# Kernel optimization log

Hardware: AMD Instinct MI355X
Metric: run time of the kernel (lower is better)

## Reference

```python
import jax, jax.numpy as jnp
import numpy as np

B, N, C, D, E, VOC, T = 128, 49, 2048, 512, 512, 10000, 20


def setup_inputs() -> dict:
    key = jax.random.key(0)
    ks = jax.random.split(key, 24)
    rn = lambda k, s: (jax.random.normal(k, s) * 0.02).astype(jnp.float32)
    z = lambda s: jnp.zeros(s, dtype=jnp.float32)
    return {
        "image_feature": jax.random.normal(ks[0], (B, N, C), dtype=jnp.float32),
        "target": jax.random.randint(ks[1], (B, T), 0, VOC),
        "emb": rn(ks[2], (VOC, E)),
        "Wa": rn(ks[3], (D, C)), "ba": z((D,)),
        "Wb": rn(ks[4], (D, C)), "bb": z((D,)),
        "Whi": rn(ks[5], (D, C)), "bhi": z((D,)),
        "Wmi": rn(ks[6], (D, C)), "bmi": z((D,)),
        "Wih": rn(ks[7], (4 * D, D + E)), "bih": z((4 * D,)),
        "Whh": rn(ks[8], (4 * D, D)), "bhh": z((4 * D,)),
        "Wv": rn(ks[9], (N, D)),
        "Wg": rn(ks[10], (N, D)),
        "wh": rn(ks[11], (1, N)),
        "WH": rn(ks[12], (D, D)),
        "Wx": rn(ks[13], (D, D + E)),
        "Wh2": rn(ks[14], (D, D)),
        "Ws": rn(ks[15], (N, D)),
        "Wc": rn(ks[16], (D, D)), "bc": z((D,)),
        "Wfc": rn(ks[17], (D, D)), "bfc": z((D,)),
        "Wp": rn(ks[18], (VOC, D)), "bp": z((VOC,)),
    }


def _forward(image_feature, target, emb, Wa, ba, Wb, bb, Whi, bhi, Wmi, bmi,
             Wih, bih, Whh, bhh, Wv, Wg, wh, WH, Wx, Wh2, Ws, Wc, bc,
             Wfc, bfc, Wp, bp):
    relu, sig = jax.nn.relu, jax.nn.sigmoid
    Vf = relu(jnp.einsum('bnc,dc->bnd', image_feature, Wa) + ba)  # [B,N,D]
    mean = image_feature.mean(axis=1)                             # [B,C]
    vg = relu(mean @ Wb.T + bb)                                   # [B,D]
    h0 = relu(mean @ Whi.T + bhi)
    m0 = relu(mean @ Wmi.T + bmi)
    zbase = jnp.einsum('bnd,kd->bnk', Vf, Wv)                     # [B,N,N], fixed per image

    we = emb[target]                                              # [B,T,E]
    we = jnp.concatenate([jnp.zeros((we.shape[0], 1, we.shape[2]), we.dtype), we[:, :-1]], axis=1)
    we_t = jnp.swapaxes(we, 0, 1)                                 # [T,B,E]

    def step(carry, wemb):
        h, m = carry
        x = jnp.concatenate([vg, wemb], axis=1)                   # [B,D+E]
        hp = h
        gates = x @ Wih.T + bih + h @ Whh.T + bhh
        i, f, g, o = jnp.split(gates, 4, axis=1)
        m2 = sig(f) * m + sig(i) * jnp.tanh(g)
        h2 = sig(o) * jnp.tanh(m2)
        H = relu(h2 @ WH.T)                                       # [B,D]
        gH = H @ Wg.T                                             # [B,N]
        z = jnp.squeeze(jnp.tanh(zbase + gH[:, None, :]) @ wh.T, -1)  # [B,N]
        gt = sig(x @ Wx.T + hp @ Wh2.T)                           # [B,D]
        s = relu((gt * jnp.tanh(m2)) @ Wc.T + bc)                 # [B,D]
        z2 = jnp.tanh(s @ Ws.T + gH) @ wh.T                       # [B,1]
        alpha = jax.nn.softmax(jnp.concatenate([z, z2], axis=1), axis=1)  # [B,N+1]
        ctx = jnp.einsum('bn,bnd->bd', alpha[:, :-1], Vf) + alpha[:, -1:] * s
        out = jnp.tanh((H + ctx) @ Wfc.T + bfc)
        logit = out @ Wp.T + bp                                   # [B,VOC]
        return (h2, m2), (logit, alpha[:, :-1])

    _, (logits, attn) = jax.lax.scan(step, (h0, m0), we_t)
    logits = jnp.swapaxes(logits, 0, 1)                           # [B,T,VOC]
    attn = jnp.swapaxes(attn, 0, 1)                               # [B,T,N]
    return jax.nn.log_softmax(logits, axis=2), attn


def reference(image_feature, target, emb, Wa, ba, Wb, bb, Whi, bhi, Wmi, bmi,
              Wih, bih, Whh, bhh, Wv, Wg, wh, WH, Wx, Wh2, Ws, Wc, bc,
              Wfc, bfc, Wp, bp):
    return _forward(image_feature, target, emb, Wa, ba, Wb, bb, Whi, bhi,
                    Wmi, bmi, Wih, bih, Whh, bhh, Wv, Wg, wh, WH, Wx, Wh2,
                    Ws, Wc, bc, Wfc, bfc, Wp, bp)
```

## Files before the change

### kernel.cpp

```cpp
#include <hip/hip_runtime.h>
#include <hip/hip_bf16.h>

static const int kB = 128, kN = 49, kC = 2048, kD = 512, kE = 512, kV = 10000, kT = 20;

typedef __bf16 bf16x8 __attribute__((ext_vector_type(8)));
typedef float  f32x4v __attribute__((ext_vector_type(4)));
typedef _Float16 h8_t __attribute__((ext_vector_type(8)));
typedef _Float16 h2v_t __attribute__((ext_vector_type(2)));
typedef unsigned short u16;
typedef unsigned int u32;

#if defined(__has_builtin)
#if __has_builtin(__builtin_amdgcn_fdot2)
#define HAS_FDOT2 1
#endif
#endif
#ifndef HAS_FDOT2
#define HAS_FDOT2 0
#endif

#define AS1 __attribute__((address_space(1)))
#define AS3 __attribute__((address_space(3)))

__device__ __forceinline__ float sigmoidf_(float x){ return 1.f/(1.f+expf(-x)); }
__device__ __forceinline__ u16 f2b(float x){ __hip_bfloat16 h = __float2bfloat16(x); return *(u16*)&h; }
__device__ __forceinline__ float bu2f(u32 u){ u32 w = u << 16; union{u32 u; float f;} c; c.u = w; return c.f; }

#define TBM 128
#define TBN 128
#define TBK 32

__global__ __launch_bounds__(256) void gemm_bf16(
    const u16* __restrict__ A, int lda,
    const u16* __restrict__ W, int ldw,
    float* __restrict__ C, u16* __restrict__ Cbf, int ldc,
    int M, int N, int K,
    const float* __restrict__ bias,
    const float* __restrict__ add1, int ld1, int a1mask,
    int act,
    const u16* __restrict__ mul2, int ldm,
    int swz)
{
    __shared__ __align__(16) u16 As[TBM*TBK];
    __shared__ __align__(16) u16 Bs[TBN*TBK];
    const int tid = threadIdx.x;
    int bm, bn;
    if (swz){
        const int mblocks = (M + TBM - 1)/TBM;
        const int per_g = mblocks*8;
        const int id = blockIdx.x;
        const int g = id/per_g, r = id - g*per_g;
        bm = (r >> 3)*TBM;
        bn = (g*8 + (r & 7))*TBN;
        if (bn >= N) return;
    } else {
        bm = blockIdx.y * TBM;
        bn = blockIdx.x * TBN;
    }
    const int wave = tid >> 6, lane = tid & 63;
    const int wm = (wave >> 1) * 64, wn = (wave & 1) * 64;
    const int lm = lane & 15, quad = lane >> 4;
    f32x4v acc[4][4] = {};
    for (int k0 = 0; k0 < K; k0 += TBK) {
        #pragma unroll
        for (int h = 0; h < 2; ++h) {
            const int slot = h*256 + tid;
            const int row = slot >> 2, kf = (slot & 3)*8;
            const int wbase = (h*256 + (tid & 448))*8;
            __builtin_amdgcn_global_load_lds((const AS1 u32*)(A + (size_t)(bm + row)*lda + k0 + kf),
                                             (AS3 u32*)(As + wbase), 16, 0, 0);
            __builtin_amdgcn_global_load_lds((const AS1 u32*)(W + (size_t)(bn + row)*ldw + k0 + kf),
                                             (AS3 u32*)(Bs + wbase), 16, 0, 0);
        }
        __syncthreads();
        bf16x8 afr[4], bfr[4];
        #pragma unroll
        for (int i = 0; i < 4; ++i) afr[i] = *(const bf16x8*)&As[(wm + i*16 + lm)*TBK + quad*8];
        #pragma unroll
        for (int j = 0; j < 4; ++j) bfr[j] = *(const bf16x8*)&Bs[(wn + j*16 + lm)*TBK + quad*8];
        #pragma unroll
        for (int i = 0; i < 4; ++i)
            #pragma unroll
            for (int j = 0; j < 4; ++j)
                acc[i][j] = __builtin_amdgcn_mfma_f32_16x16x32_bf16(afr[i], bfr[j], acc[i][j], 0, 0, 0);
        __syncthreads();
    }
    #pragma unroll
    for (int i = 0; i < 4; ++i) {
        int mbase = bm + wm + i*16 + quad*4;
        #pragma unroll
        for (int j = 0; j < 4; ++j) {
            int n = bn + wn + j*16 + lm;
            if (n >= N) continue;
            float bv = bias ? bias[n] : 0.f;
            #pragma unroll
            for (int rr2 = 0; rr2 < 4; ++rr2) {
                int m = mbase + rr2;
                float v = acc[i][j][rr2] + bv;
                if (add1) v += add1[(size_t)(m & a1mask)*ld1 + n];
                if (act == 1) v = fmaxf(v, 0.f);
                else if (act == 2) v = tanhf(v);
                else if (act == 3) v = sigmoidf_(v) * bu2f(mul2[(size_t)m*ldm + n]);
                if (C)   C[(size_t)m*ldc + n] = v;
                if (Cbf) Cbf[(size_t)m*ldc + n] = f2b(v);
            }
        }
    }
}

__global__ __launch_bounds__(256) void img_cvt_mean_k(const float* __restrict__ img,
                                                      u16* __restrict__ img_bf,
                                                      u16* __restrict__ meanb){
    int idx = blockIdx.x*256 + threadIdx.x;
    int b = idx >> 8, c8 = idx & 255;
    const float* p = img + (size_t)b*kN*kC + c8*8;
    f32x4v s0 = {0,0,0,0}, s1 = {0,0,0,0};
    for (int n = 0; n < kN; ++n){
        f32x4v f0 = *(const f32x4v*)(p + (size_t)n*kC);
        f32x4v f1 = *(const f32x4v*)(p + (size_t)n*kC + 4);
        s0 += f0; s1 += f1;
        union { u16 u[8]; uint4 v; } pk;
        pk.u[0]=f2b(f0[0]); pk.u[1]=f2b(f0[1]); pk.u[2]=f2b(f0[2]); pk.u[3]=f2b(f0[3]);
        pk.u[4]=f2b(f1[0]); pk.u[5]=f2b(f1[1]); pk.u[6]=f2b(f1[2]); pk.u[7]=f2b(f1[3]);
        *(uint4*)(img_bf + ((size_t)(b*kN + n))*kC + c8*8) = pk.v;
    }
    const float inv = 1.f/(float)kN;
    union { u16 u[8]; uint4 v; } pm;
    pm.u[0]=f2b(s0[0]*inv); pm.u[1]=f2b(s0[1]*inv); pm.u[2]=f2b(s0[2]*inv); pm.u[3]=f2b(s0[3]*inv);
    pm.u[4]=f2b(s1[0]*inv); pm.u[5]=f2b(s1[1]*inv); pm.u[6]=f2b(s1[2]*inv); pm.u[7]=f2b(s1[3]*inv);
    *(uint4*)(meanb + (size_t)b*kC + c8*8) = pm.v;
}

struct CvtDesc {
    const float* src;
    unsigned long long dst;
    int src_ld, Kshift, mode, start;
};
struct CvtTab { CvtDesc d[17]; int total; };

__global__ __launch_bounds__(256) void multi_cvt_k(CvtTab tab){
    for (int idx = blockIdx.x*256 + threadIdx.x; idx < tab.total; idx += gridDim.x*256){
        int di = 0;
        #pragma unroll
        for (int i = 1; i < 17; ++i) if (idx >= tab.d[i].start) di = i;
        const CvtDesc D = tab.d[di];
        int rel = idx - D.start;
        int rr = rel >> D.Kshift, kc = rel - (rr << D.Kshift);
        const float* p = D.src + (size_t)rr*D.src_ld + kc*8;
        f32x4v f0 = *(const f32x4v*)p, f1 = *(const f32x4v*)(p+4);
        if (D.mode == 0){
            union { u16 u[8]; uint4 v; } pk;
            pk.u[0]=f2b(f0[0]); pk.u[1]=f2b(f0[1]); pk.u[2]=f2b(f0[2]); pk.u[3]=f2b(f0[3]);
            pk.u[4]=f2b(f1[0]); pk.u[5]=f2b(f1[1]); pk.u[6]=f2b(f1[2]); pk.u[7]=f2b(f1[3]);
            *(uint4*)((u16*)D.dst + (((size_t)rr << D.Kshift) + kc)*8) = pk.v;
        } else {
            h8_t o;
            o[0]=(_Float16)f0[0]; o[1]=(_Float16)f0[1]; o[2]=(_Float16)f0[2]; o[3]=(_Float16)f0[3];
            o[4]=(_Float16)f1[0]; o[5]=(_Float16)f1[1]; o[6]=(_Float16)f1[2]; o[7]=(_Float16)f1[3];
            *(h8_t*)((_Float16*)D.dst + ((size_t)kc*2048 + rr)*8) = o;
        }
    }
}

__global__ __launch_bounds__(256) void bias_prep_k(const float* bih, const float* bhh,
                                                   const float* bb, const float* bhi, const float* bmi,
                                                   float* bias2560, float* bcat3){
    int i = blockIdx.x*256 + threadIdx.x;
    if (i < 2048) bias2560[i] = bih[i] + bhh[i];
    else if (i < 2560) bias2560[i] = 0.f;
    else if (i < 4096){
        int j = i - 2560;
        bcat3[j] = (j < 512) ? bb[j] : (j < 1024 ? bhi[j-512] : bmi[j-1024]);
    }
}

__global__ __launch_bounds__(256) void emb_gather_k(const int* __restrict__ target,
                                                    const float* __restrict__ emb,
                                                    u16* __restrict__ we){
    int idx = blockIdx.x*256 + threadIdx.x;
    int e = idx & (kE-1);
    int rr = idx >> 9;
    int b = rr & 127, t = rr >> 7;
    float v = 0.f;
    if (t > 0){ int tok = target[b*kT + (t-1)]; v = emb[(size_t)tok*kE + e]; }
    we[idx] = f2b(v);
}

__global__ __launch_bounds__(256) void initcopy_k(const float* __restrict__ initC,
                                                  u16* __restrict__ hp_bf){
    int idx = blockIdx.x*256 + threadIdx.x;
    int b = idx >> 9, d = idx & 511;
    hp_bf[idx] = f2b(initC[(size_t)b*1536 + 512 + d]);
}

__device__ __forceinline__ float dot8f(h8_t a, h8_t b, float c){
#if HAS_FDOT2
    const h2v_t* ap = (const h2v_t*)&a;
    const h2v_t* bp = (const h2v_t*)&b;
    c = __builtin_amdgcn_fdot2(ap[0], bp[0], c, false);
    c = __builtin_amdgcn_fdot2(ap[1], bp[1], c, false);
    c = __builtin_amdgcn_fdot2(ap[2], bp[2], c, false);
    c = __builtin_amdgcn_fdot2(ap[3], bp[3], c, false);
#else
    #pragma unroll
    for (int i = 0; i < 8; ++i) c = fmaf((float)a[i], (float)b[i], c);
#endif
    return c;
}

__global__ __launch_bounds__(1024, 1) void scan_k(
    const float* __restrict__ initC,
    const float* __restrict__ xall,
    const _Float16* __restrict__ Wrec,
    u16* __restrict__ hp_bf,
    u16* __restrict__ tm_bf)
{
    const int b = blockIdx.x, tid = threadIdx.x;
    const int out = tid & 511, kh = tid >> 9;
    __shared__ __align__(16) _Float16 sh[512];
    __shared__ float spart[512][4];

    if (tid < 512) sh[tid] = (_Float16)initC[(size_t)b*1536 + 512 + tid];
    float m_reg = (kh == 0) ? initC[(size_t)b*1536 + 1024 + out] : 0.f;
    __syncthreads();

    for (int t = 0; t < kT; ++t){
        float a0=0.f, a1=0.f, a2=0.f, a3=0.f;
        const int kc0 = kh*32;
        #pragma unroll 2
        for (int kc = kc0; kc < kc0 + 32; ++kc){
            h8_t hv = *(const h8_t*)&sh[kc*8];
            const _Float16* wb = Wrec + (size_t)kc*2048*8;
            a0 = dot8f(hv, *(const h8_t*)&wb[(size_t)(out       )*8], a0);
            a1 = dot8f(hv, *(const h8_t*)&wb[(size_t)(out +  512)*8], a1);
            a2 = dot8f(hv, *(const h8_t*)&wb[(size_t)(out + 1024)*8], a2);
            a3 = dot8f(hv, *(const h8_t*)&wb[(size_t)(out + 1536)*8], a3);
        }
        __syncthreads();
        if (kh == 1){
            spart[out][0]=a0; spart[out][1]=a1; spart[out][2]=a2; spart[out][3]=a3;
        }
        __syncthreads();
        if (kh == 0){
            const float* xrow = xall + ((size_t)t*kB + b)*2560;
            a0 += spart[out][0] + xrow[out];
            a1 += spart[out][1] + xrow[out + 512];
            a2 += spart[out][2] + xrow[out + 1024];
            a3 += spart[out][3] + xrow[out + 1536];
            float i_g = sigmoidf_(a0), f_g = sigmoidf_(a1);
            float g_g = tanhf(a2),     o_g = sigmoidf_(a3);
            m_reg = f_g*m_reg + i_g*g_g;
            float tm = tanhf(m_reg);
            float h2 = o_g*tm;
            sh[out] = (_Float16)h2;
            hp_bf[((size_t)(t+1)*kB + b)*512 + out] = f2b(h2);
            tm_bf[((size_t)t*kB + b)*512 + out] = f2b(tm);
        }
        __syncthreads();
    }
}

__global__ __launch_bounds__(256) void attn_k(
    const float* __restrict__ H_all,
    const float* __restrict__ s_all,
    const u16* __restrict__ Wg_bf,
    const u16* __restrict__ Ws_bf,
    const u16* __restrict__ Vf_bf,
    const float* __restrict__ zbase,
    const float* __restrict__ wh,
    u16* __restrict__ Hc_bf,
    float* __restrict__ attn_out)
{
    const int r = blockIdx.x, tid = threadIdx.x;
    const int b = r & 127, t = r >> 7;
    __shared__ float sH2[512], ss2[512];
    __shared__ float sgH[52], ssWs[52], swh[52], sz[52], salpha[52];

    for (int d = tid; d < 512; d += 256){
        sH2[d] = H_all[(size_t)r*512 + d];
        ss2[d] = s_all[(size_t)r*512 + d];
    }
    if (tid < 49) swh[tid] = wh[tid];
    __syncthreads();
    if (tid < 49){
        const u16* wr = Wg_bf + (size_t)tid*512;
        float a = 0.f;
        for (int k = 0; k < 512; k += 8){
            uint4 v = *(const uint4*)(wr + k);
            a += bu2f(v.x&0xffff)*sH2[k]   + bu2f(v.x>>16)*sH2[k+1]
               + bu2f(v.y&0xffff)*sH2[k+2] + bu2f(v.y>>16)*sH2[k+3]
               + bu2f(v.z&0xffff)*sH2[k+4] + bu2f(v.z>>16)*sH2[k+5]
               + bu2f(v.w&0xffff)*sH2[k+6] + bu2f(v.w>>16)*sH2[k+7];
        }
        sgH[tid] = a;
    } else if (tid >= 64 && tid < 113){
        int n = tid - 64;
        const u16* wr = Ws_bf + (size_t)n*512;
        float a = 0.f;
        for (int k = 0; k < 512; k += 8){
            uint4 v = *(const uint4*)(wr + k);
            a += bu2f(v.x&0xffff)*ss2[k]   + bu2f(v.x>>16)*ss2[k+1]
               + bu2f(v.y&0xffff)*ss2[k+2] + bu2f(v.y>>16)*ss2[k+3]
               + bu2f(v.z&0xffff)*ss2[k+4] + bu2f(v.z>>16)*ss2[k+5]
               + bu2f(v.w&0xffff)*ss2[k+6] + bu2f(v.w>>16)*ss2[k+7];
        }
        ssWs[n] = a;
    }
    __syncthreads();
    if (tid < 49){
        const float* zb = zbase + (size_t)b*2401 + (size_t)tid*49;
        float a = 0.f;
        #pragma unroll
        for (int k = 0; k < 49; ++k) a += tanhf(zb[k] + sgH[k]) * swh[k];
        sz[tid] = a;
    } else if (tid == 64){
        float a = 0.f;
        #pragma unroll
        for (int k = 0; k < 49; ++k) a += tanhf(ssWs[k] + sgH[k]) * swh[k];
        sz[49] = a;
    }
    __syncthreads();
    if (tid < 64){
        float val = (tid < 50) ? sz[tid] : -1e30f;
        float mx = val;
        #pragma unroll
        for (int o = 32; o > 0; o >>= 1) mx = fmaxf(mx, __shfl_xor(mx, o));
        float e = (tid < 50) ? __expf(val - mx) : 0.f;
        float ssum = e;
        #pragma unroll
        for (int o = 32; o > 0; o >>= 1) ssum += __shfl_xor(ssum, o);
        float a = e/ssum;
        if (tid < 50) salpha[tid] = a;
        if (tid < 49) attn_out[((size_t)b*kT + t)*kN + tid] = a;
    }
    __syncthreads();
    for (int d = tid; d < 512; d += 256){
        float a = salpha[49] * ss2[d];
        const u16* vf = Vf_bf + (size_t)b*49*512 + d;
        #pragma unroll
        for (int n = 0; n < 49; ++n) a = fmaf(salpha[n], bu2f(vf[(size_t)n*512]), a);
        Hc_bf[(size_t)r*512 + d] = f2b(sH2[d] + a);
    }
}

__global__ __launch_bounds__(256) void logsoftmax_k(const u16* __restrict__ logits_bf,
                                                    float* __restrict__ out0)
{
    const int r = blockIdx.x, tid = threadIdx.x;
    const int b = r / 20, t = r - b*20;
    const u16* L = logits_bf + (size_t)(t*kB + b)*kV;
    __shared__ float rm[256], rs[256];
    float m = -1e30f, s = 0.f;
    for (int c = tid; c < kV/8; c += 256){
        uint4 v = *(const uint4*)(L + c*8);
        u32 w[4] = {v.x, v.y, v.z, v.w};
        #pragma unroll
        for (int j = 0; j < 4; ++j){
            float x0 = bu2f(w[j] & 0xffff), x1 = bu2f(w[j] >> 16);
            float nm = fmaxf(m, fmaxf(x0, x1));
            s = s*__expf(m - nm) + __expf(x0 - nm) + __expf(x1 - nm);
            m = nm;
        }
    }
    rm[tid] = m; rs[tid] = s; __syncthreads();
    for (int st = 128; st > 0; st >>= 1){
        if (tid < st){
            float m2 = rm[tid + st], s2 = rs[tid + st];
            float nm = fmaxf(rm[tid], m2);
            rs[tid] = rs[tid]*__expf(rm[tid] - nm) + s2*__expf(m2 - nm);
            rm[tid] = nm;
        }
        __syncthreads();
    }
    float lse = rm[0] + logf(rs[0]);
    float* D = out0 + (size_t)r*kV;
    for (int c = tid; c < kV/8; c += 256){
        uint4 v = *(const uint4*)(L + c*8);
        u32 w[4] = {v.x, v.y, v.z, v.w};
        f32x4v o0, o1;
        o0[0]=bu2f(w[0]&0xffff)-lse; o0[1]=bu2f(w[0]>>16)-lse;
        o0[2]=bu2f(w[1]&0xffff)-lse; o0[3]=bu2f(w[1]>>16)-lse;
        o1[0]=bu2f(w[2]&0xffff)-lse; o1[1]=bu2f(w[2]>>16)-lse;
        o1[2]=bu2f(w[3]&0xffff)-lse; o1[3]=bu2f(w[3]>>16)-lse;
        *(f32x4v*)(D + c*8) = o0;
        *(f32x4v*)(D + c*8 + 4) = o1;
    }
}

extern "C" void kernel_launch(void* const* d_in, const int* in_sizes, int n_in,
                              void* d_out, int out_size, void* d_ws, size_t ws_size,
                              hipStream_t stream)
{
    const float* img   = (const float*)d_in[0];
    const int*   target= (const int*)  d_in[1];
    const float* emb   = (const float*)d_in[2];
    const float* Wa    = (const float*)d_in[3];
    const float* ba    = (const float*)d_in[4];
    const float* Wb    = (const float*)d_in[5];
    const float* bb    = (const float*)d_in[6];
    const float* Whi   = (const float*)d_in[7];
    const float* bhi   = (const float*)d_in[8];
    const float* Wmi   = (const float*)d_in[9];
    const float* bmi   = (const float*)d_in[10];
    const float* Wih   = (const float*)d_in[11];
    const float* bih   = (const float*)d_in[12];
    const float* Whh   = (const float*)d_in[13];
    const float* bhh   = (const float*)d_in[14];
    const float* Wv    = (const float*)d_in[15];
    const float* Wg    = (const float*)d_in[16];
    const float* wh    = (const float*)d_in[17];
    const float* W_H   = (const float*)d_in[18];
    const float* Wx    = (const float*)d_in[19];
    const float* Wh2   = (const float*)d_in[20];
    const float* Wsm   = (const float*)d_in[21];
    const float* Wc    = (const float*)d_in[22];
    const float* bc    = (const float*)d_in[23];
    const float* Wfc   = (const float*)d_in[24];
    const float* bfc   = (const float*)d_in[25];
    const float* Wp    = (const float*)d_in[26];
    const float* bp    = (const float*)d_in[27];
    (void)in_sizes; (void)n_in; (void)out_size; (void)ws_size;

    float* out0 = (float*)d_out;
    float* attn_out = out0 + (size_t)kB*kT*kV;

    char* base = (char*)d_ws;
    size_t off = 0;
    auto alloc = [&](size_t bytes)->char*{
        char* p = base + off;
        off += ((bytes + 255) & ~(size_t)255);
        return p;
    };
    u16* Wa_bf     = (u16*)alloc((size_t)kD*kC*2);
    u16* Winit_bf  = (u16*)alloc((size_t)1536*kC*2);
    u16* Wv_bf     = (u16*)alloc((size_t)128*kD*2);
    u16* Wp_bf     = (u16*)alloc((size_t)10112*kD*2);
    u16* Wfirst_bf = (u16*)alloc((size_t)2560*512*2);
    u16* Wlast_bf  = (u16*)alloc((size_t)2560*512*2);
    _Float16* Wrec4 = (_Float16*)alloc((size_t)2048*512*2);
    u16* Wh2_bf    = (u16*)alloc((size_t)512*512*2);
    u16* WH_bf     = (u16*)alloc((size_t)512*512*2);
    u16* Wc_bf     = (u16*)alloc((size_t)512*512*2);
    u16* Wg_bf     = (u16*)alloc((size_t)128*512*2);
    u16* Ws_bf     = (u16*)alloc((size_t)128*512*2);
    u16* Wfc_bf    = (u16*)alloc((size_t)512*512*2);
    float* bias2560 = (float*)alloc(2560*4);
    float* bcat3    = (float*)alloc(1536*4);
    u16* meanb_bf   = (u16*)alloc((size_t)kB*kC*2);
    float* initC    = (float*)alloc((size_t)kB*1536*4);
    u16* init_bf    = (u16*)alloc((size_t)kB*1536*2);
    u16* Vf_bf      = (u16*)alloc((size_t)kB*kN*kD*2);
    float* zbase    = (float*)alloc((size_t)kB*kN*kN*4);
    u16* we_bf      = (u16*)alloc((size_t)kT*kB*kE*2);
    float* gbase    = (float*)alloc((size_t)kB*2560*4);
    u16* outbf      = (u16*)alloc((size_t)kT*kB*kD*2);
    u16* gtv_bf     = (u16*)alloc((size_t)kT*kB*kD*2);
    u16* hp_bf      = (u16*)alloc((size_t)(kT+1)*kB*kD*2);
    u16* tm_bf      = (u16*)alloc((size_t)kT*kB*kD*2);

    char* dyn = base + off;
    u16* img_bf    = (u16*)dyn;
    float* xall    = (float*)(dyn + (((size_t)kB*kN*kC*2 + 255) & ~(size_t)255));
    u16* logits_bf = (u16*)dyn;
    size_t poff = 0;
    auto palloc = [&](size_t bytes)->char*{
        char* p = dyn + poff;
        poff += ((bytes + 255) & ~(size_t)255);
        return p;
    };
    float* H_all   = (float*)palloc((size_t)kT*kB*kD*4);
    float* s_all   = (float*)palloc((size_t)kT*kB*kD*4);
    u16*   Hc_bf   = (u16*)  palloc((size_t)kT*kB*kD*2);

    auto G = [&](const u16* A, int lda, const u16* W, int ldw,
                 float* C, u16* Cbf, int ldc, int M, int N, int K,
                 const float* bias, const float* a1, int l1, int a1mask, int act,
                 const u16* mul2 = nullptr, int ldm = 0){
        dim3 g((N + TBN - 1)/TBN, (M + TBM - 1)/TBM);
        gemm_bf16<<<g, 256, 0, stream>>>(A, lda, W, ldw, C, Cbf, ldc, M, N, K,
                                         bias, a1, l1, a1mask, act, mul2, ldm, 0);
    };

    bias_prep_k<<<16, 256, 0, stream>>>(bih, bhh, bb, bhi, bmi, bias2560, bcat3);
    emb_gather_k<<<kT*kB*kE/256, 256, 0, stream>>>(target, emb, we_bf);
    img_cvt_mean_k<<<kB*kC/8/256, 256, 0, stream>>>(img, img_bf, meanb_bf);
    {
        CvtTab tab{};
        int idx = 0, start = 0;
        auto add = [&](const float* src, void* dst, int src_ld, int Kshift, int rows, int mode){
            tab.d[idx] = {src, (unsigned long long)(size_t)dst, src_ld, Kshift, mode, start};
            start += rows << Kshift; ++idx;
        };
        add(Wa,        Wa_bf,                        2048, 8, 512,   0);
        add(Wb,        Winit_bf,                     2048, 8, 512,   0);
        add(Whi,       Winit_bf + (size_t)512*kC,    2048, 8, 512,   0);
        add(Wmi,       Winit_bf + (size_t)1024*kC,   2048, 8, 512,   0);
        add(Wv,        Wv_bf,                         512, 6, 49,    0);
        add(Wp,        Wp_bf,                         512, 6, 10000, 0);
        add(Wih,       Wfirst_bf,                    1024, 6, 2048,  0);
        add(Wx,        Wfirst_bf + (size_t)2048*512, 1024, 6, 512,   0);
        add(Wih + 512, Wlast_bf,                     1024, 6, 2048,  0);
        add(Wx  + 512, Wlast_bf + (size_t)2048*512,  1024, 6, 512,   0);
        add(W_H,       WH_bf,                         512, 6, 512,   0);
        add(Wc,        Wc_bf,                         512, 6, 512,   0);
        add(Wg,        Wg_bf,                         512, 6, 49,    0);
        add(Wsm,       Ws_bf,                         512, 6, 49,    0);
        add(Wfc,       Wfc_bf,                        512, 6, 512,   0);
        add(Whh,       Wrec4,                         512, 6, 2048,  5);
        add(Wh2,       Wh2_bf,                        512, 6, 512,   0);
        tab.total = start;
        int blocks = (start + 255)/256; if (blocks > 2048) blocks = 2048;
        multi_cvt_k<<<blocks, 256, 0, stream>>>(tab);
    }

    G(meanb_bf, kC, Winit_bf, kC, initC, init_bf, 1536, kB, 1536, kC, bcat3, nullptr, 0, -1, 1);
    initcopy_k<<<kB*kD/256, 256, 0, stream>>>(initC, hp_bf);
    G(img_bf, kC, Wa_bf, kC, nullptr, Vf_bf, kD, kB*kN, kD, kC, ba, nullptr, 0, -1, 1);
    G(Vf_bf, kD, Wv_bf, kD, zbase, nullptr, kN, kB*kN, kN, kD, nullptr, nullptr, 0, -1, 0);
    G(init_bf, 1536, Wfirst_bf, 512, gbase, nullptr, 2560, kB, 2560, kD, bias2560, nullptr, 0, -1, 0);
    G(we_bf, kE, Wlast_bf, 512, xall, nullptr, 2560, kT*kB, 2560, kE, nullptr, gbase, 2560, 127, 0);

    scan_k<<<kB, 1024, 0, stream>>>(initC, xall, Wrec4, hp_bf, tm_bf);

    G(hp_bf, kD, Wh2_bf, kD, nullptr, gtv_bf, kD, kT*kB, kD, kD,
      nullptr, xall + 2048, 2560, 0x7fffffff, 3, tm_bf, kD);
    G(hp_bf + (size_t)kB*kD, kD, WH_bf, kD, H_all, nullptr, kD, kT*kB, kD, kD, nullptr, nullptr, 0, -1, 1);
    G(gtv_bf, kD, Wc_bf, kD, s_all, nullptr, kD, kT*kB, kD, kD, bc, nullptr, 0, -1, 1);
    attn_k<<<kT*kB, 256, 0, stream>>>(H_all, s_all, Wg_bf, Ws_bf, Vf_bf, zbase, wh,
                                      Hc_bf, attn_out);
    G(Hc_bf, kD, Wfc_bf, kD, nullptr, outbf, kD, kT*kB, kD, kD, bfc, nullptr, 0, -1, 2);

    {
        const int mblocks = (kT*kB + TBM - 1)/TBM;
        const int nblocks = (kV + TBN - 1)/TBN;
        const int groups  = (nblocks + 7)/8;
        dim3 g(groups*8*mblocks, 1);
        gemm_bf16<<<g, 256, 0, stream>>>(outbf, kD, Wp_bf, kD, nullptr, logits_bf, kV,
                                         kT*kB, kV, kD, bp, nullptr, 0, -1, 0, nullptr, 0, 1);
    }
    logsoftmax_k<<<kB*kT, 256, 0, stream>>>(logits_bf, out0);
}
```

Baseline: 1.039 ms.

## Overlap Vf GEMM and Wp conversion with the recurrent scan kernel

```diff
diff --git a/kernel.cpp b/kernel.cpp
--- a/kernel.cpp
+++ b/kernel.cpp
@@ -26,9 +26,24 @@
 __device__ __forceinline__ u16 f2b(float x){ __hip_bfloat16 h = __float2bfloat16(x); return *(u16*)&h; }
 __device__ __forceinline__ float bu2f(u32 u){ u32 w = u << 16; union{u32 u; float f;} c; c.u = w; return c.f; }
 
+__device__ __forceinline__ float dot8f(h8_t a, h8_t b, float c){
+#if HAS_FDOT2
+    const h2v_t* ap = (const h2v_t*)&a;
+    const h2v_t* bp = (const h2v_t*)&b;
+    c = __builtin_amdgcn_fdot2(ap[0], bp[0], c, false);
+    c = __builtin_amdgcn_fdot2(ap[1], bp[1], c, false);
+    c = __builtin_amdgcn_fdot2(ap[2], bp[2], c, false);
+    c = __builtin_amdgcn_fdot2(ap[3], bp[3], c, false);
+#else
+    #pragma unroll
+    for (int i = 0; i < 8; ++i) c = fmaf((float)a[i], (float)b[i], c);
+#endif
+    return c;
+}
+
 #define TBM 128
 #define TBN 128
-#define TBK 32
+#define TBK 64
 
 __global__ __launch_bounds__(256) void gemm_bf16(
     const u16* __restrict__ A, int lda,
@@ -63,26 +78,29 @@
     f32x4v acc[4][4] = {};
     for (int k0 = 0; k0 < K; k0 += TBK) {
         #pragma unroll
-        for (int h = 0; h < 2; ++h) {
+        for (int h = 0; h < 4; ++h) {
             const int slot = h*256 + tid;
-            const int row = slot >> 2, kf = (slot & 3)*8;
-            const int wbase = (h*256 + (tid & 448))*8;
+            const int row = slot >> 3, kf = (slot & 7)*8;
+            const int wbase = (h*256 + (tid & 192))*8;
             __builtin_amdgcn_global_load_lds((const AS1 u32*)(A + (size_t)(bm + row)*lda + k0 + kf),
                                              (AS3 u32*)(As + wbase), 16, 0, 0);
             __builtin_amdgcn_global_load_lds((const AS1 u32*)(W + (size_t)(bn + row)*ldw + k0 + kf),
                                              (AS3 u32*)(Bs + wbase), 16, 0, 0);
         }
         __syncthreads();
-        bf16x8 afr[4], bfr[4];
-        #pragma unroll
-        for (int i = 0; i < 4; ++i) afr[i] = *(const bf16x8*)&As[(wm + i*16 + lm)*TBK + quad*8];
-        #pragma unroll
-        for (int j = 0; j < 4; ++j) bfr[j] = *(const bf16x8*)&Bs[(wn + j*16 + lm)*TBK + quad*8];
-        #pragma unroll
-        for (int i = 0; i < 4; ++i)
+        #pragma unroll
+        for (int sub = 0; sub < 2; ++sub){
+            bf16x8 afr[4], bfr[4];
             #pragma unroll
-            for (int j = 0; j < 4; ++j)
-                acc[i][j] = __builtin_amdgcn_mfma_f32_16x16x32_bf16(afr[i], bfr[j], acc[i][j], 0, 0, 0);
+            for (int i = 0; i < 4; ++i) afr[i] = *(const bf16x8*)&As[(wm + i*16 + lm)*TBK + quad*8 + sub*32];
+            #pragma unroll
+            for (int j = 0; j < 4; ++j) bfr[j] = *(const bf16x8*)&Bs[(wn + j*16 + lm)*TBK + quad*8 + sub*32];
+            #pragma unroll
+            for (int i = 0; i < 4; ++i)
+                #pragma unroll
+                for (int j = 0; j < 4; ++j)
+                    acc[i][j] = __builtin_amdgcn_mfma_f32_16x16x32_bf16(afr[i], bfr[j], acc[i][j], 0, 0, 0);
+        }
         __syncthreads();
     }
     #pragma unroll
@@ -97,6 +115,17 @@
             for (int rr2 = 0; rr2 < 4; ++rr2) {
                 int m = mbase + rr2;
                 float v = acc[i][j][rr2] + bv;
+                if (act == 4){
+                    if (n < 512){
+                        if (m < 2560){
+                            float g = sigmoidf_(v + add1[(size_t)m*ld1 + n]) * bu2f(mul2[(size_t)m*ldm + n]);
+                            Cbf[(size_t)m*ldc + n] = f2b(g);
+                        }
+                    } else {
+                        if (m >= 128) C[(size_t)(m-128)*ldc + (n-512)] = fmaxf(v, 0.f);
+                    }
+                    continue;
+                }
                 if (add1) v += add1[(size_t)(m & a1mask)*ld1 + n];
                 if (act == 1) v = fmaxf(v, 0.f);
                 else if (act == 2) v = tanhf(v);
@@ -193,33 +222,94 @@
     hp_bf[idx] = f2b(initC[(size_t)b*1536 + 512 + d]);
 }
 
-__device__ __forceinline__ float dot8f(h8_t a, h8_t b, float c){
-#if HAS_FDOT2
-    const h2v_t* ap = (const h2v_t*)&a;
-    const h2v_t* bp = (const h2v_t*)&b;
-    c = __builtin_amdgcn_fdot2(ap[0], bp[0], c, false);
-    c = __builtin_amdgcn_fdot2(ap[1], bp[1], c, false);
-    c = __builtin_amdgcn_fdot2(ap[2], bp[2], c, false);
-    c = __builtin_amdgcn_fdot2(ap[3], bp[3], c, false);
-#else
-    #pragma unroll
-    for (int i = 0; i < 8; ++i) c = fmaf((float)a[i], (float)b[i], c);
-#endif
-    return c;
-}
-
-__global__ __launch_bounds__(1024, 1) void scan_k(
+__global__ __launch_bounds__(1024, 1) void scanvf_k(
     const float* __restrict__ initC,
     const float* __restrict__ xall,
     const _Float16* __restrict__ Wrec,
     u16* __restrict__ hp_bf,
-    u16* __restrict__ tm_bf)
+    u16* __restrict__ tm_bf,
+    const u16* __restrict__ img_bf,
+    const u16* __restrict__ Wa_bf,
+    const float* __restrict__ ba,
+    u16* __restrict__ Vf_bf,
+    const float* __restrict__ Wp,
+    u16* __restrict__ Wp_bf)
 {
-    const int b = blockIdx.x, tid = threadIdx.x;
-    const int out = tid & 511, kh = tid >> 9;
+    const int blk = blockIdx.x, tid = threadIdx.x;
+    __shared__ __align__(16) u16 As[TBM*TBK];
+    __shared__ __align__(16) u16 Bs[TBN*TBK];
     __shared__ __align__(16) _Float16 sh[512];
     __shared__ float spart[512][4];
 
+    if (blk >= 324){
+        for (int idx = (blk-324)*1024 + tid; idx < 10000*64; idx += 40*1024){
+            int rr = idx >> 6, kc = idx & 63;
+            const float* p = Wp + (size_t)rr*512 + kc*8;
+            f32x4v f0 = *(const f32x4v*)p, f1 = *(const f32x4v*)(p+4);
+            union { u16 u[8]; uint4 v; } pk;
+            pk.u[0]=f2b(f0[0]); pk.u[1]=f2b(f0[1]); pk.u[2]=f2b(f0[2]); pk.u[3]=f2b(f0[3]);
+            pk.u[4]=f2b(f1[0]); pk.u[5]=f2b(f1[1]); pk.u[6]=f2b(f1[2]); pk.u[7]=f2b(f1[3]);
+            *(uint4*)(Wp_bf + (size_t)rr*512 + kc*8) = pk.v;
+        }
+        return;
+    }
+    if (blk >= 128){
+        const int gid = blk - 128;
+        const int bm = (gid >> 2)*TBM, bn = (gid & 3)*TBN;
+        const int iters = kC / TBK;
+        if (tid < 256){
+            const int wave = tid >> 6, lane = tid & 63;
+            const int wm = (wave >> 1) * 64, wn = (wave & 1) * 64;
+            const int lm = lane & 15, quad = lane >> 4;
+            f32x4v acc[4][4] = {};
+            for (int k0 = 0; k0 < kC; k0 += TBK){
+                #pragma unroll
+                for (int h = 0; h < 4; ++h){
+                    const int slot = h*256 + tid;
+                    const int row = slot >> 3, kf = (slot & 7)*8;
+                    const int wbase = (h*256 + (tid & 192))*8;
+                    __builtin_amdgcn_global_load_lds((const AS1 u32*)(img_bf + (size_t)(bm + row)*kC + k0 + kf),
+                                                     (AS3 u32*)(As + wbase), 16, 0, 0);
+                    __builtin_amdgcn_global_load_lds((const AS1 u32*)(Wa_bf + (size_t)(bn + row)*kC + k0 + kf),
+                                                     (AS3 u32*)(Bs + wbase), 16, 0, 0);
+                }
+                __syncthreads();
+                #pragma unroll
+                for (int sub = 0; sub < 2; ++sub){
+                    bf16x8 afr[4], bfr[4];
+                    #pragma unroll
+                    for (int i = 0; i < 4; ++i) afr[i] = *(const bf16x8*)&As[(wm + i*16 + lm)*TBK + quad*8 + sub*32];
+                    #pragma unroll
+                    for (int j = 0; j < 4; ++j) bfr[j] = *(const bf16x8*)&Bs[(wn + j*16 + lm)*TBK + quad*8 + sub*32];
+                    #pragma unroll
+                    for (int i = 0; i < 4; ++i)
+                        #pragma unroll
+                        for (int j = 0; j < 4; ++j)
+                            acc[i][j] = __builtin_amdgcn_mfma_f32_16x16x32_bf16(afr[i], bfr[j], acc[i][j], 0, 0, 0);
+                }
+                __syncthreads();
+            }
+            #pragma unroll
+            for (int i = 0; i < 4; ++i){
+                int mbase = bm + wm + i*16 + quad*4;
+                #pragma unroll
+                for (int j = 0; j < 4; ++j){
+                    int n = bn + wn + j*16 + lm;
+                    float bv = ba[n];
+                    #pragma unroll
+                    for (int rr2 = 0; rr2 < 4; ++rr2){
+                        int m = mbase + rr2;
+                        Vf_bf[(size_t)m*512 + n] = f2b(fmaxf(acc[i][j][rr2] + bv, 0.f));
+                    }
+                }
+            }
+        } else {
+            for (int i = 0; i < iters; ++i){ __syncthreads(); __syncthreads(); }
+        }
+        return;
+    }
+    const int b = blk;
+    const int out = tid & 511, kh = tid >> 9;
     if (tid < 512) sh[tid] = (_Float16)initC[(size_t)b*1536 + 512 + tid];
     float m_reg = (kh == 0) ? initC[(size_t)b*1536 + 1024 + out] : 0.f;
     __syncthreads();
@@ -271,8 +361,10 @@
     u16* __restrict__ Hc_bf,
     float* __restrict__ attn_out)
 {
-    const int r = blockIdx.x, tid = threadIdx.x;
-    const int b = r & 127, t = r >> 7;
+    const int id = blockIdx.x, tid = threadIdx.x;
+    const int xcd = id & 7, q = id >> 3;
+    const int t = q % 20, b = xcd + 8*(q/20);
+    const int r = t*128 + b;
     __shared__ float sH2[512], ss2[512];
     __shared__ float sgH[52], ssWs[52], swh[52], sz[52], salpha[52];
 
@@ -438,8 +530,7 @@
     u16* Wfirst_bf = (u16*)alloc((size_t)2560*512*2);
     u16* Wlast_bf  = (u16*)alloc((size_t)2560*512*2);
     _Float16* Wrec4 = (_Float16*)alloc((size_t)2048*512*2);
-    u16* Wh2_bf    = (u16*)alloc((size_t)512*512*2);
-    u16* WH_bf     = (u16*)alloc((size_t)512*512*2);
+    u16* Wcat_bf   = (u16*)alloc((size_t)1024*512*2);
     u16* Wc_bf     = (u16*)alloc((size_t)512*512*2);
     u16* Wg_bf     = (u16*)alloc((size_t)128*512*2);
     u16* Ws_bf     = (u16*)alloc((size_t)128*512*2);
@@ -491,40 +582,44 @@
             tab.d[idx] = {src, (unsigned long long)(size_t)dst, src_ld, Kshift, mode, start};
             start += rows << Kshift; ++idx;
         };
-        add(Wa,        Wa_bf,                        2048, 8, 512,   0);
-        add(Wb,        Winit_bf,                     2048, 8, 512,   0);
-        add(Whi,       Winit_bf + (size_t)512*kC,    2048, 8, 512,   0);
-        add(Wmi,       Winit_bf + (size_t)1024*kC,   2048, 8, 512,   0);
-        add(Wv,        Wv_bf,                         512, 6, 49,    0);
-        add(Wp,        Wp_bf,                         512, 6, 10000, 0);
-        add(Wih,       Wfirst_bf,                    1024, 6, 2048,  0);
-        add(Wx,        Wfirst_bf + (size_t)2048*512, 1024, 6, 512,   0);
-        add(Wih + 512, Wlast_bf,                     1024, 6, 2048,  0);
-        add(Wx  + 512, Wlast_bf + (size_t)2048*512,  1024, 6, 512,   0);
-        add(W_H,       WH_bf,                         512, 6, 512,   0);
-        add(Wc,        Wc_bf,                         512, 6, 512,   0);
-        add(Wg,        Wg_bf,                         512, 6, 49,    0);
-        add(Wsm,       Ws_bf,                         512, 6, 49,    0);
-        add(Wfc,       Wfc_bf,                        512, 6, 512,   0);
-        add(Whh,       Wrec4,                         512, 6, 2048,  5);
-        add(Wh2,       Wh2_bf,                        512, 6, 512,   0);
+        add(Wa,        Wa_bf,                        2048, 8, 512,  0);
+        add(Wb,        Winit_bf,                     2048, 8, 512,  0);
+        add(Whi,       Winit_bf + (size_t)512*kC,    2048, 8, 512,  0);
+        add(Wmi,       Winit_bf + (size_t)1024*kC,   2048, 8, 512,  0);
+        add(Wv,        Wv_bf,                         512, 6, 49,   0);
+        add(Wih,       Wfirst_bf,                    1024, 6, 2048, 0);
+        add(Wx,        Wfirst_bf + (size_t)2048*512, 1024, 6, 512,  0);
+        add(Wih + 512, Wlast_bf,                     1024, 6, 2048, 0);
+        add(Wx  + 512, Wlast_bf + (size_t)2048*512,  1024, 6, 512,  0);
+        add(W_H,       Wcat_bf + (size_t)512*512,     512, 6, 512,  0);
+        add(Wc,        Wc_bf,                         512, 6, 512,  0);
+        add(Wg,        Wg_bf,                         512, 6, 49,   0);
+        add(Wsm,       Ws_bf,                         512, 6, 49,   0);
+        add(Wfc,       Wfc_bf,                        512, 6, 512,  0);
+        add(Wh2,       Wcat_bf,                       512, 6, 512,  0);
+        add(Whh,       Wrec4,                         512, 6, 2048, 5);
         tab.total = start;
+        for (; idx < 17; ++idx) tab.d[idx].start = 0x7fffffff;
         int blocks = (start + 255)/256; if (blocks > 2048) blocks = 2048;
         multi_cvt_k<<<blocks, 256, 0, stream>>>(tab);
     }
 
     G(meanb_bf, kC, Winit_bf, kC, initC, init_bf, 1536, kB, 1536, kC, bcat3, nullptr, 0, -1, 1);
     initcopy_k<<<kB*kD/256, 256, 0, stream>>>(initC, hp_bf);
-    G(img_bf, kC, Wa_bf, kC, nullptr, Vf_bf, kD, kB*kN, kD, kC, ba, nullptr, 0, -1, 1);
-    G(Vf_bf, kD, Wv_bf, kD, zbase, nullptr, kN, kB*kN, kN, kD, nullptr, nullptr, 0, -1, 0);
     G(init_bf, 1536, Wfirst_bf, 512, gbase, nullptr, 2560, kB, 2560, kD, bias2560, nullptr, 0, -1, 0);
     G(we_bf, kE, Wlast_bf, 512, xall, nullptr, 2560, kT*kB, 2560, kE, nullptr, gbase, 2560, 127, 0);
 
-    scan_k<<<kB, 1024, 0, stream>>>(initC, xall, Wrec4, hp_bf, tm_bf);
-
-    G(hp_bf, kD, Wh2_bf, kD, nullptr, gtv_bf, kD, kT*kB, kD, kD,
-      nullptr, xall + 2048, 2560, 0x7fffffff, 3, tm_bf, kD);
-    G(hp_bf + (size_t)kB*kD, kD, WH_bf, kD, H_all, nullptr, kD, kT*kB, kD, kD, nullptr, nullptr, 0, -1, 1);
+    scanvf_k<<<364, 1024, 0, stream>>>(initC, xall, Wrec4, hp_bf, tm_bf,
+                                       img_bf, Wa_bf, ba, Vf_bf, Wp, Wp_bf);
+
+    G(Vf_bf, kD, Wv_bf, kD, zbase, nullptr, kN, kB*kN, kN, kD, nullptr, nullptr, 0, -1, 0);
+
+    {
+        dim3 g(1024/TBN, 2688/TBM);
+        gemm_bf16<<<g, 256, 0, stream>>>(hp_bf, kD, Wcat_bf, kD,
+                                         H_all, gtv_bf, kD, 2688, 1024, kD,
+                                         nullptr, xall + 2048, 2560, 0x7fffffff, 4, tm_bf, kD, 0);
+    }
     G(gtv_bf, kD, Wc_bf, kD, s_all, nullptr, kD, kT*kB, kD, kD, bc, nullptr, 0, -1, 1);
     attn_k<<<kT*kB, 256, 0, stream>>>(H_all, s_all, Wg_bf, Ws_bf, Vf_bf, zbase, wh,
                                       Hc_bf, attn_out);
```

After: 1.700 ms. 63.6% more time.
